# Optimization experiments

Measured on AMD Instinct MI355X. Metric: run time of the kernel, lower is better.

## Reference

```python
import jax, jax.numpy as jnp
import numpy as np

# ---- configuration (matches init_kwargs) ----
IH, IW, IC, OC = 32, 32, 8, 16
KH = KW = 3
STRIDE = (1, 1)
PAD = (1, 1)
DIL = (1, 1)
P = 5                       # num_gp_pts per GP neuron
I_DIM = IC * KH * KW        # 72 = kernel_input_size
OH = (IH + 2 * PAD[0] - DIL[0] * (KH - 1) - 1) // STRIDE[0] + 1
OW = (IW + 2 * PAD[1] - DIL[1] * (KW - 1) - 1) // STRIDE[1] + 1
JITTER = 1e-4


def setup_inputs() -> dict:
    key = jax.random.key(0)
    k1, k2, k3, k4, k5 = jax.random.split(key, 5)
    N = 8
    x_mean = jax.random.normal(k1, (N, IH, IW, IC), jnp.float32)
    # variances must be positive
    x_var = 0.1 + 0.9 * jax.random.uniform(k2, (N, IH, IW, IC), jnp.float32)
    # inducing inputs: spread on [-1,1] with small perturbation (well-conditioned K)
    base = jnp.linspace(-1.0, 1.0, P, dtype=jnp.float32)
    z = base[None, None, :] + 0.05 * jax.random.normal(k3, (OC, I_DIM, P), jnp.float32)
    h = jax.random.normal(k4, (OC, I_DIM, P), jnp.float32)      # inducing outputs
    raw_l = jax.random.uniform(k5, (OC, I_DIM), jnp.float32)    # pre-softplus lengthscale
    return {"x_mean": x_mean, "x_var": x_var, "z": z, "h": h, "raw_l": raw_l}


def im2col(img):
    """[N,IH,IW,C] NHWC -> [N*L, C*KH*KW], torch.nn.Unfold ordering (channel slowest)."""
    x = jnp.transpose(img, (0, 3, 1, 2))  # NCHW, matches the torch transposes
    patches = jax.lax.conv_general_dilated_patches(
        x, (KH, KW), STRIDE, [(PAD[0], PAD[0]), (PAD[1], PAD[1])], rhs_dilation=DIL
    )  # [N, C*KH*KW, OH, OW], feature dim channel-major like torch unfold
    Nb = patches.shape[0]
    return patches.reshape(Nb, I_DIM, OH * OW).transpose(0, 2, 1).reshape(Nb * OH * OW, I_DIM)


def gp_layer(mu, s2, z, h, raw_l):
    """GP-neuron (KAN-style) moment propagation.
    mu, s2: [R, I]; z, h: [O, I, P]; raw_l: [O, I].
    Per neuron (o,i): SE kernel k(a,b)=exp(-(a-b)^2/(2 l^2)), unit signal variance.
    Under x_i ~ N(mu_i, s2_i):
      q_p   = sqrt(l^2/(l^2+s2)) * exp(-(mu-z_p)^2 / (2 (l^2+s2)))   (expected kernel)
      mean  = q . K^{-1} h
      var   = 1 - q . K^{-1} q
    Layer output (KAN sum over inputs): y_o = sum_i f_oi(x_i).
    """
    l2 = jax.nn.softplus(raw_l) ** 2                                  # [O,I]
    dz = z[:, :, :, None] - z[:, :, None, :]                          # [O,I,P,P]
    K = jnp.exp(-0.5 * dz**2 / l2[:, :, None, None]) + JITTER * jnp.eye(P, dtype=mu.dtype)
    Kinv = jnp.linalg.inv(K)                                          # [O,I,P,P] (tiny)
    alpha = jnp.einsum('oipq,oiq->oip', Kinv, h)                      # [O,I,P]

    d = l2[None, :, :, None] + s2[:, None, :, None]                   # [R,O,I,1]
    diff = mu[:, None, :, None] - z[None]                             # [R,O,I,P]
    q = jnp.sqrt(l2[None, :, :, None] / d) * jnp.exp(-0.5 * diff**2 / d)  # [R,O,I,P]

    out_mean = jnp.einsum('roip,oip->ro', q, alpha)                   # [R,O]
    qK = jnp.einsum('roip,oipq->roiq', q, Kinv)                       # [R,O,I,P]
    qKq = jnp.einsum('roiq,roiq->ro', qK, q)                          # [R,O]
    # sum_i (k(x,x) - q K^{-1} q) with k(x,x)=1 -> I - sum_i qKq_i
    out_var = jnp.maximum(jnp.asarray(mu.shape[1], mu.dtype) - qKq, 1e-6)
    return out_mean, out_var


def reference(x_mean, x_var, z, h, raw_l):
    N = x_mean.shape[0]
    mu = im2col(x_mean)                  # [N*L, I]
    s2 = im2col(x_var)                   # [N*L, I]
    m, v = gp_layer(mu, s2, z, h, raw_l)
    # col2im: [N*L, OC] -> [N, OH, OW, OC]
    return m.reshape(N, OH, OW, OC), v.reshape(N, OH, OW, OC)
```

## Files before the change

kernel.cpp:

```cpp
#include <hip/hip_runtime.h>
#include <math.h>

#define OC_N   16
#define I_DIM  72
#define PN     5
#define NEU    (OC_N * I_DIM)
#define NF     32
#define RTOT   8192
#define OUT_HALF (RTOT * OC_N)
#define LOG2E  1.4426950408889634f
#define RLOG2E 0.6931471805599453f

#if __has_builtin(__builtin_amdgcn_rcpf)
#define RCPF(x) __builtin_amdgcn_rcpf(x)
#else
#define RCPF(x) (1.0f / (x))
#endif
#if __has_builtin(__builtin_amdgcn_exp2f)
#define EXP2F(x) __builtin_amdgcn_exp2f(x)
#else
#define EXP2F(x) exp2f(x)
#endif
#if __has_builtin(__builtin_amdgcn_logf)
#define LOG2F(x) __builtin_amdgcn_logf(x)
#else
#define LOG2F(x) log2f(x)
#endif


__global__ __launch_bounds__(256) void gp_prep_kernel(
    const float* __restrict__ zin, const float* __restrict__ hin,
    const float* __restrict__ rlin, float* __restrict__ nr) {
  int idx = blockIdx.x * blockDim.x + threadIdx.x;
  if (idx >= NEU) return;
  float x  = rlin[idx];
  float t  = EXP2F(-fabsf(x) * LOG2E);
  float sp = fmaxf(x, 0.0f) + LOG2F(1.0f + t) * RLOG2E;
  float l2 = sp * sp;
  float cexp = -0.5f * LOG2E * RCPF(l2);

  float zz[PN], hh[PN];
#pragma unroll
  for (int p = 0; p < PN; ++p) {
    zz[p] = zin[idx * PN + p];
    hh[p] = hin[idx * PN + p];
  }
  float A[PN][PN], B[PN][PN];
#pragma unroll
  for (int p = 0; p < PN; ++p) {
#pragma unroll
    for (int q = 0; q < PN; ++q) {
      float dz = zz[p] - zz[q];
      A[p][q] = EXP2F(cexp * dz * dz);
      B[p][q] = (p == q) ? 1.0f : 0.0f;
    }
  }
#pragma unroll
  for (int p = 0; p < PN; ++p) A[p][p] += 1e-4f;

#pragma unroll
  for (int c = 0; c < PN; ++c) {
    float pivinv = RCPF(A[c][c]);
#pragma unroll
    for (int j = 0; j < PN; ++j) { A[c][j] *= pivinv; B[c][j] *= pivinv; }
#pragma unroll
    for (int r = 0; r < PN; ++r) {
      if (r == c) continue;
      float f = A[r][c];
#pragma unroll
      for (int j = 0; j < PN; ++j) { A[r][j] -= f * A[c][j]; B[r][j] -= f * B[c][j]; }
    }
  }
  float alpha[PN];
#pragma unroll
  for (int p = 0; p < PN; ++p) {
    float s = 0.0f;
#pragma unroll
    for (int q = 0; q < PN; ++q) s += B[p][q] * hh[q];
    alpha[p] = s;
  }
  float* o = nr + idx * NF;
  o[0] = l2;
  o[1] = 0.0f;
#pragma unroll
  for (int p = 0; p < PN; ++p) {
    o[2 + p]  = zz[p];
    o[7 + p]  = alpha[p];
    o[12 + p] = B[p][p];
  }
  int j = 17;
#pragma unroll
  for (int p = 0; p < PN; ++p)
#pragma unroll
    for (int q = p + 1; q < PN; ++q) o[j++] = 2.0f * B[p][q];
  o[27] = o[28] = o[29] = o[30] = o[31] = 0.0f;
}

template <int TPS>
__global__ __launch_bounds__(256) void gp_main_kernel(
    const float* __restrict__ xm, const float* __restrict__ xv,
    const float* __restrict__ nr, float2* __restrict__ pmq) {
  const int o   = blockIdx.y;
  const int seg = blockIdx.z;
  const int r = blockIdx.x * 256 + threadIdx.x;
  const int n  = r >> 10;
  const int pix = r & 1023;
  const int oh = pix >> 5;
  const int ow = pix & 31;
  const float* nb = nr + o * (I_DIM * NF);

  float mean_acc = 0.0f;
  float qkq_acc  = 0.0f;

#pragma unroll
  for (int j = 0; j < TPS; ++j) {
    const int k  = seg * TPS + j;
    const int kh = k / 3;
    const int kw = k - kh * 3;
    const int ih = oh + kh - 1;
    const int iw = ow + kw - 1;
    const bool vld = ((unsigned)ih < 32u) & ((unsigned)iw < 32u);
    float mu[8], s2[8];
    if (vld) {
      const int base = ((n * 32 + ih) * 32 + iw) * 8;
      const float4 a0 = *(const float4*)(xm + base);
      const float4 a1 = *(const float4*)(xm + base + 4);
      const float4 b0 = *(const float4*)(xv + base);
      const float4 b1 = *(const float4*)(xv + base + 4);
      mu[0]=a0.x; mu[1]=a0.y; mu[2]=a0.z; mu[3]=a0.w;
      mu[4]=a1.x; mu[5]=a1.y; mu[6]=a1.z; mu[7]=a1.w;
      s2[0]=b0.x; s2[1]=b0.y; s2[2]=b0.z; s2[3]=b0.w;
      s2[4]=b1.x; s2[5]=b1.y; s2[6]=b1.z; s2[7]=b1.w;
    } else {
#pragma unroll
      for (int c = 0; c < 8; ++c) { mu[c] = 0.0f; s2[c] = 0.0f; }
    }
#pragma unroll
    for (int c = 0; c < 8; ++c) {
      const float* p = nb + (c * 9 + k) * NF;
      const float l2    = p[0];
      const float d     = l2 + s2[c];
      const float inv_d = RCPF(d);
      const float coef2 = l2 * inv_d;
      const float coef  = sqrtf(coef2);
      const float el    = -0.72134752044f * inv_d;
      const float m     = mu[c];
      const float d0 = m - p[2];
      const float d1 = m - p[3];
      const float d2 = m - p[4];
      const float d3 = m - p[5];
      const float d4 = m - p[6];
      const float u0 = EXP2F(el * d0 * d0);
      const float u1 = EXP2F(el * d1 * d1);
      const float u2 = EXP2F(el * d2 * d2);
      const float u3 = EXP2F(el * d3 * d3);
      const float u4 = EXP2F(el * d4 * d4);
      const float dotA =
          fmaf(u0, p[7], fmaf(u1, p[8], fmaf(u2, p[9], fmaf(u3, p[10], u4 * p[11]))));
      const float t0 = fmaf(p[12], u0, fmaf(p[17], u1, fmaf(p[18], u2, fmaf(p[19], u3, p[20] * u4))));
      const float t1 = fmaf(p[13], u1, fmaf(p[21], u2, fmaf(p[22], u3, p[23] * u4)));
      const float t2 = fmaf(p[14], u2, fmaf(p[24], u3, p[25] * u4));
      const float t3 = fmaf(p[15], u3, p[26] * u4);
      const float t4 = p[16] * u4;
      const float quad =
          fmaf(u0, t0, fmaf(u1, t1, fmaf(u2, t2, fmaf(u3, t3, u4 * t4))));
      mean_acc = fmaf(coef, dotA, mean_acc);
      qkq_acc  = fmaf(coef2, quad, qkq_acc);
    }
  }
  pmq[(seg * OC_N + o) * RTOT + r] = make_float2(mean_acc, qkq_acc);
}

template <int SEGS>
__global__ __launch_bounds__(256) void gp_final_kernel(
    const float2* __restrict__ pmq, float* __restrict__ out) {
  const int j = blockIdx.x * 256 + threadIdx.x;
  const int o = j >> 13;
  const int r = j & 8191;
  float m = 0.0f, q = 0.0f;
#pragma unroll
  for (int s = 0; s < SEGS; ++s) {
    const float2 v = pmq[(s * OC_N + o) * RTOT + r];
    m += v.x;
    q += v.y;
  }
  const int i = r * OC_N + o;
  out[i] = m;
  out[OUT_HALF + i] = fmaxf(72.0f - q, 1e-6f);
}

extern "C" void kernel_launch(void* const* d_in, const int* in_sizes, int n_in,
                              void* d_out, int out_size, void* d_ws, size_t ws_size,
                              hipStream_t stream) {
  const float* xm = (const float*)d_in[0];
  const float* xv = (const float*)d_in[1];
  const float* z  = (const float*)d_in[2];
  const float* h  = (const float*)d_in[3];
  const float* rl = (const float*)d_in[4];
  float* out = (float*)d_out;

  float* nr   = (float*)d_ws;
  float2* pmq = (float2*)((char*)d_ws + NEU * NF * 4);
  const size_t need9 = (size_t)NEU * NF * 4 + (size_t)9 * OC_N * RTOT * 8;

  gp_prep_kernel<<<dim3((NEU + 255) / 256), dim3(256), 0, stream>>>(z, h, rl, nr);

  if (ws_size >= need9) {
    dim3 grid(RTOT / 256, OC_N, 9);
    gp_main_kernel<1><<<grid, dim3(256), 0, stream>>>(xm, xv, nr, pmq);
    gp_final_kernel<9><<<dim3(OUT_HALF / 256), dim3(256), 0, stream>>>(pmq, out);
  } else {
    dim3 grid(RTOT / 256, OC_N, 3);
    gp_main_kernel<3><<<grid, dim3(256), 0, stream>>>(xm, xv, nr, pmq);
    gp_final_kernel<3><<<dim3(OUT_HALF / 256), dim3(256), 0, stream>>>(pmq, out);
  }
}
```

Baseline: 88.05 us.

## Fuse main and final kernels via in-block shared-memory reduction over kernel taps

Replaces the split main kernel plus separate reduction kernel with one fused kernel whose 64x9 block assigns one kernel tap per wavefront and reduces the nine partial sums through shared memory. This removes the global partial-sum buffer round-trip and one kernel launch. The trade-offs are a block-wide barrier, only one of nine wavefronts doing the final write, and 576-thread blocks that may limit occupancy.

```diff
diff --git a/kernel.cpp b/kernel.cpp
--- a/kernel.cpp
+++ b/kernel.cpp
@@ -96,97 +96,92 @@
   o[27] = o[28] = o[29] = o[30] = o[31] = 0.0f;
 }
 
-template <int TPS>
-__global__ __launch_bounds__(256) void gp_main_kernel(
+__global__ __launch_bounds__(576) void gp_fused_kernel(
     const float* __restrict__ xm, const float* __restrict__ xv,
-    const float* __restrict__ nr, float2* __restrict__ pmq) {
-  const int o   = blockIdx.y;
-  const int seg = blockIdx.z;
-  const int r = blockIdx.x * 256 + threadIdx.x;
+    const float* __restrict__ nr, float* __restrict__ out) {
+  const int tx = threadIdx.x;
+  const int k  = __builtin_amdgcn_readfirstlane(threadIdx.y);
+  const int o  = blockIdx.y;
+  const int r  = blockIdx.x * 64 + tx;
   const int n  = r >> 10;
   const int pix = r & 1023;
   const int oh = pix >> 5;
   const int ow = pix & 31;
   const float* nb = nr + o * (I_DIM * NF);
 
+  const int kh = k / 3;
+  const int kw = k - kh * 3;
+  const int ih = oh + kh - 1;
+  const int iw = ow + kw - 1;
+  const bool vld = ((unsigned)ih < 32u) & ((unsigned)iw < 32u);
+
+  float mu[8], s2[8];
+  if (vld) {
+    const int base = ((n * 32 + ih) * 32 + iw) * 8;
+    const float4 a0 = *(const float4*)(xm + base);
+    const float4 a1 = *(const float4*)(xm + base + 4);
+    const float4 b0 = *(const float4*)(xv + base);
+    const float4 b1 = *(const float4*)(xv + base + 4);
+    mu[0]=a0.x; mu[1]=a0.y; mu[2]=a0.z; mu[3]=a0.w;
+    mu[4]=a1.x; mu[5]=a1.y; mu[6]=a1.z; mu[7]=a1.w;
+    s2[0]=b0.x; s2[1]=b0.y; s2[2]=b0.z; s2[3]=b0.w;
+    s2[4]=b1.x; s2[5]=b1.y; s2[6]=b1.z; s2[7]=b1.w;
+  } else {
+#pragma unroll
+    for (int c = 0; c < 8; ++c) { mu[c] = 0.0f; s2[c] = 0.0f; }
+  }
+
   float mean_acc = 0.0f;
   float qkq_acc  = 0.0f;
-
-#pragma unroll
-  for (int j = 0; j < TPS; ++j) {
-    const int k  = seg * TPS + j;
-    const int kh = k / 3;
-    const int kw = k - kh * 3;
-    const int ih = oh + kh - 1;
-    const int iw = ow + kw - 1;
-    const bool vld = ((unsigned)ih < 32u) & ((unsigned)iw < 32u);
-    float mu[8], s2[8];
-    if (vld) {
-      const int base = ((n * 32 + ih) * 32 + iw) * 8;
-      const float4 a0 = *(const float4*)(xm + base);
-      const float4 a1 = *(const float4*)(xm + base + 4);
-      const float4 b0 = *(const float4*)(xv + base);
-      const float4 b1 = *(const float4*)(xv + base + 4);
-      mu[0]=a0.x; mu[1]=a0.y; mu[2]=a0.z; mu[3]=a0.w;
-      mu[4]=a1.x; mu[5]=a1.y; mu[6]=a1.z; mu[7]=a1.w;
-      s2[0]=b0.x; s2[1]=b0.y; s2[2]=b0.z; s2[3]=b0.w;
-      s2[4]=b1.x; s2[5]=b1.y; s2[6]=b1.z; s2[7]=b1.w;
-    } else {
-#pragma unroll
-      for (int c = 0; c < 8; ++c) { mu[c] = 0.0f; s2[c] = 0.0f; }
+#pragma unroll
+  for (int c = 0; c < 8; ++c) {
+    const float* p = nb + (c * 9 + k) * NF;
+    const float l2    = p[0];
+    const float d     = l2 + s2[c];
+    const float inv_d = RCPF(d);
+    const float coef2 = l2 * inv_d;
+    const float coef  = sqrtf(coef2);
+    const float el    = -0.72134752044f * inv_d;
+    const float m     = mu[c];
+    const float d0 = m - p[2];
+    const float d1 = m - p[3];
+    const float d2 = m - p[4];
+    const float d3 = m - p[5];
+    const float d4 = m - p[6];
+    const float u0 = EXP2F(el * d0 * d0);
+    const float u1 = EXP2F(el * d1 * d1);
+    const float u2 = EXP2F(el * d2 * d2);
+    const float u3 = EXP2F(el * d3 * d3);
+    const float u4 = EXP2F(el * d4 * d4);
+    const float dotA =
+        fmaf(u0, p[7], fmaf(u1, p[8], fmaf(u2, p[9], fmaf(u3, p[10], u4 * p[11]))));
+    const float t0 = fmaf(p[12], u0, fmaf(p[17], u1, fmaf(p[18], u2, fmaf(p[19], u3, p[20] * u4))));
+    const float t1 = fmaf(p[13], u1, fmaf(p[21], u2, fmaf(p[22], u3, p[23] * u4)));
+    const float t2 = fmaf(p[14], u2, fmaf(p[24], u3, p[25] * u4));
+    const float t3 = fmaf(p[15], u3, p[26] * u4);
+    const float t4 = p[16] * u4;
+    const float quad =
+        fmaf(u0, t0, fmaf(u1, t1, fmaf(u2, t2, fmaf(u3, t3, u4 * t4))));
+    mean_acc = fmaf(coef, dotA, mean_acc);
+    qkq_acc  = fmaf(coef2, quad, qkq_acc);
+  }
+
+  __shared__ float2 red[9][64];
+  red[threadIdx.y][tx] = make_float2(mean_acc, qkq_acc);
+  __syncthreads();
+  if (threadIdx.y == 0) {
+    float m = mean_acc;
+    float q = qkq_acc;
+#pragma unroll
+    for (int s = 1; s < 9; ++s) {
+      const float2 v = red[s][tx];
+      m += v.x;
+      q += v.y;
     }
-#pragma unroll
-    for (int c = 0; c < 8; ++c) {
-      const float* p = nb + (c * 9 + k) * NF;
-      const float l2    = p[0];
-      const float d     = l2 + s2[c];
-      const float inv_d = RCPF(d);
-      const float coef2 = l2 * inv_d;
-      const float coef  = sqrtf(coef2);
-      const float el    = -0.72134752044f * inv_d;
-      const float m     = mu[c];
-      const float d0 = m - p[2];
-      const float d1 = m - p[3];
-      const float d2 = m - p[4];
-      const float d3 = m - p[5];
-      const float d4 = m - p[6];
-      const float u0 = EXP2F(el * d0 * d0);
-      const float u1 = EXP2F(el * d1 * d1);
-      const float u2 = EXP2F(el * d2 * d2);
-      const float u3 = EXP2F(el * d3 * d3);
-      const float u4 = EXP2F(el * d4 * d4);
-      const float dotA =
-          fmaf(u0, p[7], fmaf(u1, p[8], fmaf(u2, p[9], fmaf(u3, p[10], u4 * p[11]))));
-      const float t0 = fmaf(p[12], u0, fmaf(p[17], u1, fmaf(p[18], u2, fmaf(p[19], u3, p[20] * u4))));
-      const float t1 = fmaf(p[13], u1, fmaf(p[21], u2, fmaf(p[22], u3, p[23] * u4)));
-      const float t2 = fmaf(p[14], u2, fmaf(p[24], u3, p[25] * u4));
-      const float t3 = fmaf(p[15], u3, p[26] * u4);
-      const float t4 = p[16] * u4;
-      const float quad =
-          fmaf(u0, t0, fmaf(u1, t1, fmaf(u2, t2, fmaf(u3, t3, u4 * t4))));
-      mean_acc = fmaf(coef, dotA, mean_acc);
-      qkq_acc  = fmaf(coef2, quad, qkq_acc);
-    }
-  }
-  pmq[(seg * OC_N + o) * RTOT + r] = make_float2(mean_acc, qkq_acc);
-}
-
-template <int SEGS>
-__global__ __launch_bounds__(256) void gp_final_kernel(
-    const float2* __restrict__ pmq, float* __restrict__ out) {
-  const int j = blockIdx.x * 256 + threadIdx.x;
-  const int o = j >> 13;
-  const int r = j & 8191;
-  float m = 0.0f, q = 0.0f;
-#pragma unroll
-  for (int s = 0; s < SEGS; ++s) {
-    const float2 v = pmq[(s * OC_N + o) * RTOT + r];
-    m += v.x;
-    q += v.y;
-  }
-  const int i = r * OC_N + o;
-  out[i] = m;
-  out[OUT_HALF + i] = fmaxf(72.0f - q, 1e-6f);
+    const int i = r * OC_N + o;
+    out[i] = m;
+    out[OUT_HALF + i] = fmaxf(72.0f - q, 1e-6f);
+  }
 }
 
 extern "C" void kernel_launch(void* const* d_in, const int* in_sizes, int n_in,
@@ -198,20 +193,11 @@
   const float* h  = (const float*)d_in[3];
   const float* rl = (const float*)d_in[4];
   float* out = (float*)d_out;
-
-  float* nr   = (float*)d_ws;
-  float2* pmq = (float2*)((char*)d_ws + NEU * NF * 4);
-  const size_t need9 = (size_t)NEU * NF * 4 + (size_t)9 * OC_N * RTOT * 8;
+  float* nr  = (float*)d_ws;
 
   gp_prep_kernel<<<dim3((NEU + 255) / 256), dim3(256), 0, stream>>>(z, h, rl, nr);
 
-  if (ws_size >= need9) {
-    dim3 grid(RTOT / 256, OC_N, 9);
-    gp_main_kernel<1><<<grid, dim3(256), 0, stream>>>(xm, xv, nr, pmq);
-    gp_final_kernel<9><<<dim3(OUT_HALF / 256), dim3(256), 0, stream>>>(pmq, out);
-  } else {
-    dim3 grid(RTOT / 256, OC_N, 3);
-    gp_main_kernel<3><<<grid, dim3(256), 0, stream>>>(xm, xv, nr, pmq);
-    gp_final_kernel<3><<<dim3(OUT_HALF / 256), dim3(256), 0, stream>>>(pmq, out);
-  }
+  dim3 grid(RTOT / 64, OC_N);
+  dim3 block(64, 9);
+  gp_fused_kernel<<<grid, block, 0, stream>>>(xm, xv, nr, out);
 }
```

New measurement: 86.66 us. About the same (-1.6%).

## Split main kernel across input channels with per-lane neuron params and shuffle reduction

Applied to the files above, without the earlier changes.

The main kernel now maps each lane to one input channel and eight pixel groups. Each thread loads its neuron's 27 parameters into registers once, instead of reading them per pixel from global or cache. Partial sums over the 8 channels are combined with xor shuffles, and a single lane writes the results. This cuts repeated parameter loads and gives coalesced scalar input reads, at the cost of shuffle work, 64-thread blocks, and dropping the fallback for a small workspace.

```diff
diff --git a/kernel.cpp b/kernel.cpp
--- a/kernel.cpp
+++ b/kernel.cpp
@@ -96,82 +96,109 @@
   o[27] = o[28] = o[29] = o[30] = o[31] = 0.0f;
 }
 
-template <int TPS>
-__global__ __launch_bounds__(256) void gp_main_kernel(
+__global__ __launch_bounds__(64, 4) void gp_main_kernel(
     const float* __restrict__ xm, const float* __restrict__ xv,
     const float* __restrict__ nr, float2* __restrict__ pmq) {
-  const int o   = blockIdx.y;
-  const int seg = blockIdx.z;
-  const int r = blockIdx.x * 256 + threadIdx.x;
-  const int n  = r >> 10;
-  const int pix = r & 1023;
-  const int oh = pix >> 5;
-  const int ow = pix & 31;
-  const float* nb = nr + o * (I_DIM * NF);
-
-  float mean_acc = 0.0f;
-  float qkq_acc  = 0.0f;
-
-#pragma unroll
-  for (int j = 0; j < TPS; ++j) {
-    const int k  = seg * TPS + j;
-    const int kh = k / 3;
-    const int kw = k - kh * 3;
-    const int ih = oh + kh - 1;
-    const int iw = ow + kw - 1;
-    const bool vld = ((unsigned)ih < 32u) & ((unsigned)iw < 32u);
-    float mu[8], s2[8];
-    if (vld) {
-      const int base = ((n * 32 + ih) * 32 + iw) * 8;
-      const float4 a0 = *(const float4*)(xm + base);
-      const float4 a1 = *(const float4*)(xm + base + 4);
-      const float4 b0 = *(const float4*)(xv + base);
-      const float4 b1 = *(const float4*)(xv + base + 4);
-      mu[0]=a0.x; mu[1]=a0.y; mu[2]=a0.z; mu[3]=a0.w;
-      mu[4]=a1.x; mu[5]=a1.y; mu[6]=a1.z; mu[7]=a1.w;
-      s2[0]=b0.x; s2[1]=b0.y; s2[2]=b0.z; s2[3]=b0.w;
-      s2[4]=b1.x; s2[5]=b1.y; s2[6]=b1.z; s2[7]=b1.w;
-    } else {
-#pragma unroll
-      for (int c = 0; c < 8; ++c) { mu[c] = 0.0f; s2[c] = 0.0f; }
-    }
-#pragma unroll
-    for (int c = 0; c < 8; ++c) {
-      const float* p = nb + (c * 9 + k) * NF;
-      const float l2    = p[0];
-      const float d     = l2 + s2[c];
-      const float inv_d = RCPF(d);
-      const float coef2 = l2 * inv_d;
-      const float coef  = sqrtf(coef2);
-      const float el    = -0.72134752044f * inv_d;
-      const float m     = mu[c];
-      const float d0 = m - p[2];
-      const float d1 = m - p[3];
-      const float d2 = m - p[4];
-      const float d3 = m - p[5];
-      const float d4 = m - p[6];
-      const float u0 = EXP2F(el * d0 * d0);
-      const float u1 = EXP2F(el * d1 * d1);
-      const float u2 = EXP2F(el * d2 * d2);
-      const float u3 = EXP2F(el * d3 * d3);
-      const float u4 = EXP2F(el * d4 * d4);
-      const float dotA =
-          fmaf(u0, p[7], fmaf(u1, p[8], fmaf(u2, p[9], fmaf(u3, p[10], u4 * p[11]))));
-      const float t0 = fmaf(p[12], u0, fmaf(p[17], u1, fmaf(p[18], u2, fmaf(p[19], u3, p[20] * u4))));
-      const float t1 = fmaf(p[13], u1, fmaf(p[21], u2, fmaf(p[22], u3, p[23] * u4)));
-      const float t2 = fmaf(p[14], u2, fmaf(p[24], u3, p[25] * u4));
-      const float t3 = fmaf(p[15], u3, p[26] * u4);
-      const float t4 = p[16] * u4;
-      const float quad =
-          fmaf(u0, t0, fmaf(u1, t1, fmaf(u2, t2, fmaf(u3, t3, u4 * t4))));
-      mean_acc = fmaf(coef, dotA, mean_acc);
-      qkq_acc  = fmaf(coef2, quad, qkq_acc);
-    }
-  }
-  pmq[(seg * OC_N + o) * RTOT + r] = make_float2(mean_acc, qkq_acc);
-}
-
-template <int SEGS>
+  const int lane = threadIdx.x;
+  const int rh = lane >> 3;
+  const int c  = lane & 7;
+  const int k  = blockIdx.z;
+  const int kh = k / 3;
+  const int kw = k - kh * 3;
+  const int o  = blockIdx.y;
+  const int rbase = blockIdx.x * 128;
+  const int n = rbase >> 10;
+  const int ohb = (rbase & 1023) >> 5;
+
+  const float* rec = nr + (o * I_DIM + (c * 9 + k)) * NF;
+  float P[27];
+#pragma unroll
+  for (int j = 0; j < 27; ++j) P[j] = rec[j];
+  const float l2 = P[0];
+
+  float2 outm[8], outq[8];
+
+#pragma unroll
+  for (int it = 0; it < 8; ++it) {
+    const int oh  = ohb + (it >> 1);
+    const int ow0 = (it & 1) << 4;
+    const int ih  = oh + kh - 1;
+    const int iwa = ow0 + rh + kw - 1;
+    const int iwb = iwa + 8;
+    const bool va = ((unsigned)ih < 32u) & ((unsigned)iwa < 32u);
+    const bool vb = ((unsigned)ih < 32u) & ((unsigned)iwb < 32u);
+    const int ihc  = ih  < 0 ? 0 : (ih  > 31 ? 31 : ih);
+    const int iwac = iwa < 0 ? 0 : (iwa > 31 ? 31 : iwa);
+    const int iwbc = iwb < 0 ? 0 : (iwb > 31 ? 31 : iwb);
+    const int rowb = ((n * 32 + ihc) * 32) * 8 + c;
+    float ma  = xm[rowb + iwac * 8];
+    float mb  = xm[rowb + iwbc * 8];
+    float sa  = xv[rowb + iwac * 8];
+    float sb  = xv[rowb + iwbc * 8];
+    ma = va ? ma : 0.0f;  sa = va ? sa : 0.0f;
+    mb = vb ? mb : 0.0f;  sb = vb ? sb : 0.0f;
+
+    const float da  = l2 + sa,            db  = l2 + sb;
+    const float ia  = RCPF(da),           ib  = RCPF(db);
+    const float c2a = l2 * ia,            c2b = l2 * ib;
+    const float ca  = sqrtf(c2a),         cb  = sqrtf(c2b);
+    const float ea  = -0.72134752044f * ia, eb = -0.72134752044f * ib;
+
+    float ua0, ua1, ua2, ua3, ua4, ub0, ub1, ub2, ub3, ub4;
+    {
+      const float x0 = ma - P[2], y0 = mb - P[2];
+      const float x1 = ma - P[3], y1 = mb - P[3];
+      const float x2 = ma - P[4], y2 = mb - P[4];
+      const float x3 = ma - P[5], y3 = mb - P[5];
+      const float x4 = ma - P[6], y4 = mb - P[6];
+      ua0 = EXP2F(ea * x0 * x0);  ub0 = EXP2F(eb * y0 * y0);
+      ua1 = EXP2F(ea * x1 * x1);  ub1 = EXP2F(eb * y1 * y1);
+      ua2 = EXP2F(ea * x2 * x2);  ub2 = EXP2F(eb * y2 * y2);
+      ua3 = EXP2F(ea * x3 * x3);  ub3 = EXP2F(eb * y3 * y3);
+      ua4 = EXP2F(ea * x4 * x4);  ub4 = EXP2F(eb * y4 * y4);
+    }
+    const float dAa =
+        fmaf(ua0, P[7], fmaf(ua1, P[8], fmaf(ua2, P[9], fmaf(ua3, P[10], ua4 * P[11]))));
+    const float dAb =
+        fmaf(ub0, P[7], fmaf(ub1, P[8], fmaf(ub2, P[9], fmaf(ub3, P[10], ub4 * P[11]))));
+    const float ta0 = fmaf(P[12], ua0, fmaf(P[17], ua1, fmaf(P[18], ua2, fmaf(P[19], ua3, P[20] * ua4))));
+    const float tb0 = fmaf(P[12], ub0, fmaf(P[17], ub1, fmaf(P[18], ub2, fmaf(P[19], ub3, P[20] * ub4))));
+    const float ta1 = fmaf(P[13], ua1, fmaf(P[21], ua2, fmaf(P[22], ua3, P[23] * ua4)));
+    const float tb1 = fmaf(P[13], ub1, fmaf(P[21], ub2, fmaf(P[22], ub3, P[23] * ub4)));
+    const float ta2 = fmaf(P[14], ua2, fmaf(P[24], ua3, P[25] * ua4));
+    const float tb2 = fmaf(P[14], ub2, fmaf(P[24], ub3, P[25] * ub4));
+    const float ta3 = fmaf(P[15], ua3, P[26] * ua4);
+    const float tb3 = fmaf(P[15], ub3, P[26] * ub4);
+    const float ta4 = P[16] * ua4;
+    const float tb4 = P[16] * ub4;
+    const float qa =
+        fmaf(ua0, ta0, fmaf(ua1, ta1, fmaf(ua2, ta2, fmaf(ua3, ta3, ua4 * ta4))));
+    const float qb =
+        fmaf(ub0, tb0, fmaf(ub1, tb1, fmaf(ub2, tb2, fmaf(ub3, tb3, ub4 * tb4))));
+    float meana = ca * dAa,  meanb = cb * dAb;
+    float qkqa  = c2a * qa,  qkqb  = c2b * qb;
+
+    meana += __shfl_xor(meana, 1); meanb += __shfl_xor(meanb, 1);
+    qkqa  += __shfl_xor(qkqa, 1);  qkqb  += __shfl_xor(qkqb, 1);
+    meana += __shfl_xor(meana, 2); meanb += __shfl_xor(meanb, 2);
+    qkqa  += __shfl_xor(qkqa, 2);  qkqb  += __shfl_xor(qkqb, 2);
+    meana += __shfl_xor(meana, 4); meanb += __shfl_xor(meanb, 4);
+    qkqa  += __shfl_xor(qkqa, 4);  qkqb  += __shfl_xor(qkqb, 4);
+    outm[it] = make_float2(meana, meanb);
+    outq[it] = make_float2(qkqa, qkqb);
+  }
+
+  if (c == 0) {
+    float2* base = pmq + (size_t)(k * OC_N + o) * RTOT + rbase;
+#pragma unroll
+    for (int it = 0; it < 8; ++it) {
+      const int r0 = it * 16;
+      base[r0 + rh]     = make_float2(outm[it].x, outq[it].x);
+      base[r0 + rh + 8] = make_float2(outm[it].y, outq[it].y);
+    }
+  }
+}
+
 __global__ __launch_bounds__(256) void gp_final_kernel(
     const float2* __restrict__ pmq, float* __restrict__ out) {
   const int j = blockIdx.x * 256 + threadIdx.x;
@@ -179,8 +206,8 @@
   const int r = j & 8191;
   float m = 0.0f, q = 0.0f;
 #pragma unroll
-  for (int s = 0; s < SEGS; ++s) {
-    const float2 v = pmq[(s * OC_N + o) * RTOT + r];
+  for (int s = 0; s < 9; ++s) {
+    const float2 v = pmq[(size_t)(s * OC_N + o) * RTOT + r];
     m += v.x;
     q += v.y;
   }
@@ -201,17 +228,11 @@
 
   float* nr   = (float*)d_ws;
   float2* pmq = (float2*)((char*)d_ws + NEU * NF * 4);
-  const size_t need9 = (size_t)NEU * NF * 4 + (size_t)9 * OC_N * RTOT * 8;
 
   gp_prep_kernel<<<dim3((NEU + 255) / 256), dim3(256), 0, stream>>>(z, h, rl, nr);
 
-  if (ws_size >= need9) {
-    dim3 grid(RTOT / 256, OC_N, 9);
-    gp_main_kernel<1><<<grid, dim3(256), 0, stream>>>(xm, xv, nr, pmq);
-    gp_final_kernel<9><<<dim3(OUT_HALF / 256), dim3(256), 0, stream>>>(pmq, out);
-  } else {
-    dim3 grid(RTOT / 256, OC_N, 3);
-    gp_main_kernel<3><<<grid, dim3(256), 0, stream>>>(xm, xv, nr, pmq);
-    gp_final_kernel<3><<<dim3(OUT_HALF / 256), dim3(256), 0, stream>>>(pmq, out);
-  }
-}
+  dim3 grid(RTOT / 128, OC_N, 9);
+  gp_main_kernel<<<grid, dim3(64), 0, stream>>>(xm, xv, nr, pmq);
+
+  gp_final_kernel<<<dim3(OUT_HALF / 256), dim3(256), 0, stream>>>(pmq, out);
+}
```

Measured after the change: 94.91 us. 7.8% more time.
